# Optimization experiments

Measured on AMD Instinct MI355X. Metric: run time of the kernel, lower is better.

Reference implementation:

```python
import jax, jax.numpy as jnp
import numpy as np

L, K, V = 16, 2, 2
KV = K * V
S = 1 << L          # 65536 trellis states
R = 1 << (L - KV)   # 4096 reduced states
D = 1 << KV         # 16 candidate predecessors per state
B = 512             # viterbi batch rows


def _fp4_s1e2m1(x4):
    # x4: int array of 4-bit fp4 codes (s1e2m1, subnormal support)
    s = (x4 >> 3) & 1
    e = (x4 >> 1) & 3
    m = (x4 & 1).astype(np.float32)
    ef = e.astype(np.float32)
    val = np.where(e == 0, 0.5 * m, (1.0 + 0.5 * m) * np.exp2(ef - 1.0))
    return (val * np.where(s == 0, 1.0, -1.0)).astype(np.float32)


def _training_lut_fp4_v2():
    # CodebookLUTfreeFP4(L=16, V=2).get_training_lut()
    x = np.arange(S, dtype=np.int64)
    t = (((x + 1) * x) >> (16 - 8 - 1)) & 255   # big_index_to_small_index, 8-bit index
    pair = np.stack([(t >> 4) & 15, t & 15], axis=-1)  # int8_to_mx_pair -> [S, 2]
    lut = _fp4_s1e2m1(pair)
    return lut / lut.std(ddof=1)                 # torch .std() is unbiased


def setup_inputs() -> dict:
    key = jax.random.key(0)
    k1, k2 = jax.random.split(key)
    training_lut = jnp.asarray(_training_lut_fp4_v2(), dtype=jnp.float32)   # [S, V]
    cost = jax.random.uniform(k1, (B, S), dtype=jnp.float32) * 4.0          # running path costs
    orig_seq_part = jax.random.normal(k2, (B, V), dtype=jnp.float32)        # next V weights of each seq
    sumdelta = np.arange(D, dtype=np.int64) << (L - KV)                     # [D]
    base = (np.arange(S, dtype=np.int64) >> KV)[::D]                        # [R]
    state_candidates = jnp.asarray(base[:, None] + sumdelta[None, :], dtype=jnp.int32)  # [R, D]
    return {"training_lut": training_lut, "cost": cost,
            "orig_seq_part": orig_seq_part, "state_candidates": state_candidates}


def reference(training_lut, cost, orig_seq_part, state_candidates):
    # TrellisQuantizer.update: one Viterbi trellis transition
    Bb, Ss = cost.shape
    Rr, Dd = state_candidates.shape
    # gather candidate predecessor costs: cand_cost[b, r, d] = cost[b, state_candidates[r, d]]
    cand_cost = cost[:, state_candidates]                                   # [B, R, D]
    best_val = jnp.min(cand_cost, axis=-1)                                  # [B, R]
    best_idx = jnp.argmin(cand_cost, axis=-1)                               # [B, R]
    # squared error of every trellis state's codeword vs the observed V weights
    state_err = jnp.sum((training_lut[None, :, :] - orig_seq_part[:, None, :]) ** 2, axis=-1)  # [B, S]
    # expand best predecessor cost over the D states sharing it (view/expand/reshape in torch)
    new_cost = state_err + jnp.broadcast_to(best_val[:, :, None], (Bb, Rr, Dd)).reshape(Bb, Ss)
    # backpointer: which predecessor state won
    prev_state = state_candidates[jnp.arange(Rr)[None, :], best_idx]        # [B, R]
    return prev_state, new_cost
```

## Files before the change

kernel.cpp:

```cpp
#include <hip/hip_runtime.h>

constexpr int S_ = 1 << 16;
constexpr int R_ = 1 << 12;
constexpr int D_ = 16;
constexpr int B_ = 512;
constexpr int BLOCK = 256;
constexpr int RPB = 512;
constexpr int CHUNKS = R_ / RPB;
constexpr int TILE_FLOATS = D_ * RPB;

__global__ __launch_bounds__(256) void build_tab_kernel(
    const float* __restrict__ lut, float2* __restrict__ tab)
{
    const unsigned s = blockIdx.x * 256u + threadIdx.x;
    const unsigned t = (((s + 1u) * s) >> 7) & 255u;
    tab[t] = make_float2(lut[2 * s], lut[2 * s + 1]);
}

__global__ __launch_bounds__(BLOCK) void trellis_kernel(
    const float*  __restrict__ cost,
    const float*  __restrict__ orig,
    const float2* __restrict__ tab,
    float*        __restrict__ prev_state_out,
    float*        __restrict__ new_cost)
{
    __shared__ float tile[TILE_FLOATS];
    __shared__ float lds_bv[RPB];
    __shared__ float lds_err[256];

    const int b      = blockIdx.x / CHUNKS;
    const int rchunk = blockIdx.x % CHUNKS;
    const int r0     = rchunk * RPB;
    const int tid    = threadIdx.x;
    const int wave   = tid >> 6;
    const int lane   = tid & 63;

    const float  o0 = orig[2 * b + 0];
    const float  o1 = orig[2 * b + 1];
    const float2 tv = tab[tid];

    const float* costb = cost + (size_t)b * S_;
    #pragma unroll
    for (int j = 0; j < 8; ++j) {
        const int c    = wave * 8 + j;
        const int d    = c >> 1;
        const int half = c & 1;
        const float* g = costb + d * R_ + r0 + half * 256 + lane * 4;
        float*       l = tile + c * 256;
        __builtin_amdgcn_global_load_lds(
            (const __attribute__((address_space(1))) void*)g,
            (__attribute__((address_space(3))) void*)l,
            16, 0, 0);
    }

    {
        const float e0 = tv.x - o0, e1 = tv.y - o1;
        lds_err[tid] = e0 * e0 + e1 * e1;
    }

    __syncthreads();

    const int rl = tid * 2;
    float2 v0 = *(const float2*)(tile + rl);
    float bva = v0.x, bvb = v0.y;
    int   bia = 0,   bib = 0;
    #pragma unroll
    for (int d = 1; d < D_; ++d) {
        const float2 v = *(const float2*)(tile + d * RPB + rl);
        if (v.x < bva) { bva = v.x; bia = d; }
        if (v.y < bvb) { bvb = v.y; bib = d; }
    }
    const int rg = r0 + rl;
    *(float2*)(prev_state_out + (size_t)b * R_ + rg) =
        make_float2((float)(rg + (bia << 12)), (float)(rg + 1 + (bib << 12)));
    lds_bv[rl]     = bva;
    lds_bv[rl + 1] = bvb;
    __syncthreads();

    const int s_base = r0 * D_;
    #pragma unroll
    for (int it = 0; it < (RPB * D_) / (BLOCK * 4); ++it) {
        const int flat = it * (BLOCK * 4) + tid * 4;
        const unsigned s = (unsigned)(s_base + flat);
        const float bv = lds_bv[flat >> 4];
        float4 out;
        out.x = lds_err[(((s + 1u) * (s + 0u)) >> 7) & 255u] + bv;
        out.y = lds_err[(((s + 2u) * (s + 1u)) >> 7) & 255u] + bv;
        out.z = lds_err[(((s + 3u) * (s + 2u)) >> 7) & 255u] + bv;
        out.w = lds_err[(((s + 4u) * (s + 3u)) >> 7) & 255u] + bv;
        *(float4*)(new_cost + (size_t)b * S_ + (int)s) = out;
    }
}

extern "C" void kernel_launch(void* const* d_in, const int* in_sizes, int n_in,
                              void* d_out, int out_size, void* d_ws, size_t ws_size,
                              hipStream_t stream) {
    const float* lut  = (const float*)d_in[0];
    const float* cost = (const float*)d_in[1];
    const float* orig = (const float*)d_in[2];

    float* prev_state = (float*)d_out;
    float* new_cost   = (float*)d_out + (size_t)B_ * R_;
    float2* tab       = (float2*)d_ws;

    hipLaunchKernelGGL(build_tab_kernel, dim3(S_ / 256), dim3(256), 0, stream,
                       lut, tab);
    hipLaunchKernelGGL(trellis_kernel, dim3(B_ * CHUNKS), dim3(BLOCK), 0, stream,
                       cost, orig, tab, prev_state, new_cost);
}
```

Before: 247.6 us.

## Replace LDS-staged cost tile with direct float4 global loads per thread

Each thread now reads its four reduced states' 16 candidate costs straight from global memory with float4 loads and does the min/argmin in registers. This removes the 32 KB LDS tile, the async global-to-LDS copies and one barrier. Rows per block double from 512 to 1024, which halves the grid. A launch-bounds occupancy hint of 6 blocks per CU is added. The cost is that global-load latency is no longer overlapped through LDS staging, and fewer, larger blocks may reduce parallelism.

```diff
diff --git a/kernel.cpp b/kernel.cpp
--- a/kernel.cpp
+++ b/kernel.cpp
@@ -5,9 +5,9 @@
 constexpr int D_ = 16;
 constexpr int B_ = 512;
 constexpr int BLOCK = 256;
-constexpr int RPB = 512;
+constexpr int RPT  = 4;
+constexpr int RPB  = BLOCK * RPT;
 constexpr int CHUNKS = R_ / RPB;
-constexpr int TILE_FLOATS = D_ * RPB;
 
 __global__ __launch_bounds__(256) void build_tab_kernel(
     const float* __restrict__ lut, float2* __restrict__ tab)
@@ -17,14 +17,13 @@
     tab[t] = make_float2(lut[2 * s], lut[2 * s + 1]);
 }
 
-__global__ __launch_bounds__(BLOCK) void trellis_kernel(
+__global__ __launch_bounds__(BLOCK, 6) void trellis_kernel(
     const float*  __restrict__ cost,
     const float*  __restrict__ orig,
     const float2* __restrict__ tab,
     float*        __restrict__ prev_state_out,
     float*        __restrict__ new_cost)
 {
-    __shared__ float tile[TILE_FLOATS];
     __shared__ float lds_bv[RPB];
     __shared__ float lds_err[256];
 
@@ -32,63 +31,52 @@
     const int rchunk = blockIdx.x % CHUNKS;
     const int r0     = rchunk * RPB;
     const int tid    = threadIdx.x;
-    const int wave   = tid >> 6;
-    const int lane   = tid & 63;
 
     const float  o0 = orig[2 * b + 0];
     const float  o1 = orig[2 * b + 1];
     const float2 tv = tab[tid];
 
-    const float* costb = cost + (size_t)b * S_;
+    const int r = r0 + tid * RPT;
+    const float* pb = cost + (size_t)b * S_ + r;
+
+    float4 bv = *(const float4*)pb;
+    int bia = 0, bib = 0, bic = 0, bid_ = 0;
     #pragma unroll
-    for (int j = 0; j < 8; ++j) {
-        const int c    = wave * 8 + j;
-        const int d    = c >> 1;
-        const int half = c & 1;
-        const float* g = costb + d * R_ + r0 + half * 256 + lane * 4;
-        float*       l = tile + c * 256;
-        __builtin_amdgcn_global_load_lds(
-            (const __attribute__((address_space(1))) void*)g,
-            (__attribute__((address_space(3))) void*)l,
-            16, 0, 0);
+    for (int d = 1; d < D_; ++d) {
+        const float4 v = *(const float4*)(pb + (size_t)d * R_);
+        if (v.x < bv.x) { bv.x = v.x; bia  = d; }
+        if (v.y < bv.y) { bv.y = v.y; bib  = d; }
+        if (v.z < bv.z) { bv.z = v.z; bic  = d; }
+        if (v.w < bv.w) { bv.w = v.w; bid_ = d; }
     }
+
+    *(float4*)(prev_state_out + (size_t)b * R_ + r) =
+        make_float4((float)(r     + (bia  << 12)),
+                    (float)(r + 1 + (bib  << 12)),
+                    (float)(r + 2 + (bic  << 12)),
+                    (float)(r + 3 + (bid_ << 12)));
+
+    *(float4*)(lds_bv + tid * RPT) = bv;
 
     {
         const float e0 = tv.x - o0, e1 = tv.y - o1;
         lds_err[tid] = e0 * e0 + e1 * e1;
     }
-
     __syncthreads();
 
-    const int rl = tid * 2;
-    float2 v0 = *(const float2*)(tile + rl);
-    float bva = v0.x, bvb = v0.y;
-    int   bia = 0,   bib = 0;
-    #pragma unroll
-    for (int d = 1; d < D_; ++d) {
-        const float2 v = *(const float2*)(tile + d * RPB + rl);
-        if (v.x < bva) { bva = v.x; bia = d; }
-        if (v.y < bvb) { bvb = v.y; bib = d; }
-    }
-    const int rg = r0 + rl;
-    *(float2*)(prev_state_out + (size_t)b * R_ + rg) =
-        make_float2((float)(rg + (bia << 12)), (float)(rg + 1 + (bib << 12)));
-    lds_bv[rl]     = bva;
-    lds_bv[rl + 1] = bvb;
-    __syncthreads();
-
-    const int s_base = r0 * D_;
+    const int s_base = r0 << 4;
+    float* outb = new_cost + (size_t)b * S_ + s_base;
     #pragma unroll
     for (int it = 0; it < (RPB * D_) / (BLOCK * 4); ++it) {
         const int flat = it * (BLOCK * 4) + tid * 4;
         const unsigned s = (unsigned)(s_base + flat);
-        const float bv = lds_bv[flat >> 4];
+        const float bvv = lds_bv[flat >> 4];
         float4 out;
-        out.x = lds_err[(((s + 1u) * (s + 0u)) >> 7) & 255u] + bv;
-        out.y = lds_err[(((s + 2u) * (s + 1u)) >> 7) & 255u] + bv;
-        out.z = lds_err[(((s + 3u) * (s + 2u)) >> 7) & 255u] + bv;
-        out.w = lds_err[(((s + 4u) * (s + 3u)) >> 7) & 255u] + bv;
-        *(float4*)(new_cost + (size_t)b * S_ + (int)s) = out;
+        out.x = lds_err[(((s + 1u) * (s + 0u)) >> 7) & 255u] + bvv;
+        out.y = lds_err[(((s + 2u) * (s + 1u)) >> 7) & 255u] + bvv;
+        out.z = lds_err[(((s + 3u) * (s + 2u)) >> 7) & 255u] + bvv;
+        out.w = lds_err[(((s + 4u) * (s + 3u)) >> 7) & 255u] + bvv;
+        *(float4*)(outb + flat) = out;
     }
 }
 
```

Measured after the change: 255.4 us. 1.03x slower.

## Split trellis kernel into separate reduce and expand kernels

Applied to the files above, without the earlier changes.

Splits the fused trellis kernel into two launches. A reduce kernel computes the min and argmin over the 16 candidate predecessors and stores the best values in a scratch region at the start of each new_cost chunk. An expand kernel then reads them back and writes the expanded state error plus best cost. This presumably shortens each kernel and frees LDS and registers for better occupancy, at the cost of an extra launch and an extra global round trip for the best values.

```diff
diff --git a/kernel.cpp b/kernel.cpp
--- a/kernel.cpp
+++ b/kernel.cpp
@@ -5,9 +5,10 @@
 constexpr int D_ = 16;
 constexpr int B_ = 512;
 constexpr int BLOCK = 256;
-constexpr int RPB = 512;
+constexpr int RPB  = 512;
 constexpr int CHUNKS = R_ / RPB;
 constexpr int TILE_FLOATS = D_ * RPB;
+constexpr int SPB = RPB * D_;
 
 __global__ __launch_bounds__(256) void build_tab_kernel(
     const float* __restrict__ lut, float2* __restrict__ tab)
@@ -17,16 +18,12 @@
     tab[t] = make_float2(lut[2 * s], lut[2 * s + 1]);
 }
 
-__global__ __launch_bounds__(BLOCK) void trellis_kernel(
-    const float*  __restrict__ cost,
-    const float*  __restrict__ orig,
-    const float2* __restrict__ tab,
-    float*        __restrict__ prev_state_out,
-    float*        __restrict__ new_cost)
+__global__ __launch_bounds__(BLOCK) void reduce_kernel(
+    const float* __restrict__ cost,
+    float*       __restrict__ prev_state_out,
+    float*       __restrict__ new_cost)
 {
     __shared__ float tile[TILE_FLOATS];
-    __shared__ float lds_bv[RPB];
-    __shared__ float lds_err[256];
 
     const int b      = blockIdx.x / CHUNKS;
     const int rchunk = blockIdx.x % CHUNKS;
@@ -34,10 +31,6 @@
     const int tid    = threadIdx.x;
     const int wave   = tid >> 6;
     const int lane   = tid & 63;
-
-    const float  o0 = orig[2 * b + 0];
-    const float  o1 = orig[2 * b + 1];
-    const float2 tv = tab[tid];
 
     const float* costb = cost + (size_t)b * S_;
     #pragma unroll
@@ -52,12 +45,6 @@
             (__attribute__((address_space(3))) void*)l,
             16, 0, 0);
     }
-
-    {
-        const float e0 = tv.x - o0, e1 = tv.y - o1;
-        lds_err[tid] = e0 * e0 + e1 * e1;
-    }
-
     __syncthreads();
 
     const int rl = tid * 2;
@@ -73,22 +60,46 @@
     const int rg = r0 + rl;
     *(float2*)(prev_state_out + (size_t)b * R_ + rg) =
         make_float2((float)(rg + (bia << 12)), (float)(rg + 1 + (bib << 12)));
-    lds_bv[rl]     = bva;
-    lds_bv[rl + 1] = bvb;
+    *(float2*)(new_cost + (size_t)b * S_ + r0 * D_ + rl) =
+        make_float2(bva, bvb);
+}
+
+__global__ __launch_bounds__(BLOCK) void expand_kernel(
+    const float*  __restrict__ orig,
+    const float2* __restrict__ tab,
+    float*        __restrict__ new_cost)
+{
+    __shared__ float lds_bv[RPB];
+    __shared__ float lds_err[256];
+
+    const int b      = blockIdx.x / CHUNKS;
+    const int chunk  = blockIdx.x % CHUNKS;
+    const int s_base = chunk * SPB;
+    const int tid    = threadIdx.x;
+
+    float* rowo = new_cost + (size_t)b * S_;
+
+    *(float2*)(lds_bv + tid * 2) = *(const float2*)(rowo + s_base + tid * 2);
+
+    {
+        const float2 tv = tab[tid];
+        const float e0 = tv.x - orig[2 * b + 0];
+        const float e1 = tv.y - orig[2 * b + 1];
+        lds_err[tid] = e0 * e0 + e1 * e1;
+    }
     __syncthreads();
 
-    const int s_base = r0 * D_;
     #pragma unroll
-    for (int it = 0; it < (RPB * D_) / (BLOCK * 4); ++it) {
+    for (int it = 0; it < SPB / (BLOCK * 4); ++it) {
         const int flat = it * (BLOCK * 4) + tid * 4;
         const unsigned s = (unsigned)(s_base + flat);
-        const float bv = lds_bv[flat >> 4];
+        const float bvv = lds_bv[flat >> 4];
         float4 out;
-        out.x = lds_err[(((s + 1u) * (s + 0u)) >> 7) & 255u] + bv;
-        out.y = lds_err[(((s + 2u) * (s + 1u)) >> 7) & 255u] + bv;
-        out.z = lds_err[(((s + 3u) * (s + 2u)) >> 7) & 255u] + bv;
-        out.w = lds_err[(((s + 4u) * (s + 3u)) >> 7) & 255u] + bv;
-        *(float4*)(new_cost + (size_t)b * S_ + (int)s) = out;
+        out.x = lds_err[(((s + 1u) * (s + 0u)) >> 7) & 255u] + bvv;
+        out.y = lds_err[(((s + 2u) * (s + 1u)) >> 7) & 255u] + bvv;
+        out.z = lds_err[(((s + 3u) * (s + 2u)) >> 7) & 255u] + bvv;
+        out.w = lds_err[(((s + 4u) * (s + 3u)) >> 7) & 255u] + bvv;
+        *(float4*)(rowo + (int)s) = out;
     }
 }
 
@@ -105,6 +116,8 @@
 
     hipLaunchKernelGGL(build_tab_kernel, dim3(S_ / 256), dim3(256), 0, stream,
                        lut, tab);
-    hipLaunchKernelGGL(trellis_kernel, dim3(B_ * CHUNKS), dim3(BLOCK), 0, stream,
-                       cost, orig, tab, prev_state, new_cost);
+    hipLaunchKernelGGL(reduce_kernel, dim3(B_ * CHUNKS), dim3(BLOCK), 0, stream,
+                       cost, prev_state, new_cost);
+    hipLaunchKernelGGL(expand_kernel, dim3(B_ * CHUNKS), dim3(BLOCK), 0, stream,
+                       orig, tab, new_cost);
 }
```

Result: no change. 249.9 us (+0.9%).
